# Kernel tuning notes

Hardware: AMD Instinct MI355X
Metric: run time of the kernel (lower is better)

## Reference

```python
import jax, jax.numpy as jnp
import numpy as np

COMMITMENT_COST = 0.25

def setup_inputs() -> dict:
    key = jax.random.key(0)
    k1, k2 = jax.random.split(key)
    z = jax.random.normal(k1, (8, 2048, 768), dtype=jnp.float32)
    # codebook initialized uniform(-1/K, 1/K) in the original; use same scale
    K = 2048
    emb = jax.random.uniform(k2, (K, 768), dtype=jnp.float32, minval=-1.0 / K, maxval=1.0 / K)
    return {"z": z, "emb": emb}

def reference(z, emb):
    B, S, D = z.shape
    z_flat = z.reshape(-1, D)                                   # [N, D]
    # squared-euclidean distances via expansion: ||z||^2 + ||e||^2 - 2 z e^T
    distances = (
        jnp.sum(z_flat * z_flat, axis=1, keepdims=True)
        + jnp.sum(emb * emb, axis=1)
        - 2.0 * jnp.matmul(z_flat, emb.T)
    )                                                           # [N, K]
    ids_flat = jnp.argmin(distances, axis=1)                    # [N]
    z_q = emb[ids_flat].reshape(z.shape)                        # gather + reshape
    concept_ids = ids_flat.reshape(B, S)
    # training path with use_ema=True: codebook_loss = 0, commitment term only.
    # NOTE: original (faithfully) computes mse(z.detach(), z_q) — grad flows to z_q.
    commitment_loss = jnp.mean((jax.lax.stop_gradient(z) - z_q) ** 2)
    vq_loss = COMMITMENT_COST * commitment_loss
    # straight-through estimator
    z_q_st = z + jax.lax.stop_gradient(z_q - z)
    return z_q_st, concept_ids, vq_loss
```

## Files before the change

kernel.cpp:

```cpp
#include <hip/hip_runtime.h>
#include <float.h>

typedef unsigned short ushort_t;
typedef unsigned int uint_t;

#define NROWS 16384
#define DDIM  768
#define KCODES 2048
#define NCB2   8
#define MARGIN 8e-4f

__device__ __forceinline__ ushort_t f2bf(float x) {
    uint_t u = __float_as_uint(x);
    uint_t r = (u + 0x7fffu + ((u >> 16) & 1u)) >> 16;
    return (ushort_t)r;
}

__device__ __forceinline__ uint_t fenc(float f) {
    uint_t u = __float_as_uint(f);
    return (u & 0x80000000u) ? ~u : (u | 0x80000000u);
}
__device__ __forceinline__ float fdec(uint_t k) {
    uint_t u = (k & 0x80000000u) ? (k ^ 0x80000000u) : ~k;
    return __uint_as_float(u);
}

__global__ void prep_kernel(const float* __restrict__ z, const float* __restrict__ emb,
                            float* __restrict__ ee, float* __restrict__ zz,
                            ushort_t* __restrict__ Zh, ushort_t* __restrict__ Eh,
                            float* __restrict__ out_loss) {
    const int b = blockIdx.x, t = threadIdx.x;
    if (b == 0 && t == 0) out_loss[0] = 0.f;
    if (b < KCODES) {
        const int c = b;
        const float* e = emb + (size_t)c * DDIM;
        float s = 0.f;
        for (int i = t; i < DDIM; i += 256) { float v = e[i]; s += v * v; }
        for (int off = 32; off; off >>= 1) s += __shfl_down(s, off);
        __shared__ float red[4];
        if ((t & 63) == 0) red[t >> 6] = s;
        __syncthreads();
        if (t == 0) ee[c] = red[0] + red[1] + red[2] + red[3];
        if (t < 192) {
            const float4 v = ((const float4*)e)[t];
            ushort4 h;
            h.x = f2bf(v.x); h.y = f2bf(v.y); h.z = f2bf(v.z); h.w = f2bf(v.w);
            ((ushort4*)(Eh + (size_t)c * DDIM))[t] = h;
        }
    } else {
        const int rb = b - KCODES;
        const int row = rb * 4 + (t >> 6);
        const int lane = t & 63;
        const float* zr = z + (size_t)row * DDIM;
        float s = 0.f;
        for (int i = lane; i < DDIM; i += 64) { float v = zr[i]; s += v * v; }
        for (int off = 32; off; off >>= 1) s += __shfl_down(s, off);
        if (lane == 0) zz[row] = s;
        const float4* zr4 = (const float4*)zr;
        ushort4* dh = (ushort4*)(Zh + (size_t)row * DDIM);
        #pragma unroll
        for (int j = 0; j < 3; ++j) {
            const int i4 = lane + 64 * j;
            const float4 v = zr4[i4];
            ushort4 h;
            h.x = f2bf(v.x); h.y = f2bf(v.y); h.z = f2bf(v.z); h.w = f2bf(v.w);
            dh[i4] = h;
        }
    }
}

typedef __attribute__((ext_vector_type(8))) short bf16x8;
typedef __attribute__((ext_vector_type(4))) float f32x4;

__device__ __forceinline__ int swz(int r) { return (r & 3) ^ ((r >> 2) & 3); }

#define RINGB 24576
#define CAPS  8

__global__ __launch_bounds__(256, 2)
void mfma_ring_kernel(const ushort_t* __restrict__ Ab, const ushort_t* __restrict__ Bb,
                      const float* __restrict__ ee, float* __restrict__ bmin,
                      float2* __restrict__ slots) {
    __shared__ __align__(16) char smem[3 * RINGB];
    uint_t* rowminU = (uint_t*)smem;
    int*    rcnt    = (int*)(smem + 512);
    float (*sval)[CAPS] = (float(*)[CAPS])(smem + 1024);
    int   (*sidx)[CAPS] = (int(*)[CAPS])(smem + 5120);

    const int t = threadIdx.x;
    const int w = t >> 6, l = t & 63;
    const int bx = blockIdx.x & 127;
    const int by = blockIdx.x >> 7;
    const int row0 = bx << 7;
    const int col0 = by << 8;

    f32x4 acc[4][8];
    #pragma unroll
    for (int i = 0; i < 4; ++i)
        #pragma unroll
        for (int j = 0; j < 8; ++j) acc[i][j] = (f32x4){0.f, 0.f, 0.f, 0.f};

    const int sri = l >> 2, slot = l & 3;
    const ushort_t* gA[2]; uint_t lA[2];
    #pragma unroll
    for (int q = 0; q < 2; ++q) {
        const int r0 = ((w << 1) + q) << 4;
        const int ra = r0 + sri;
        const int c  = slot ^ swz(ra);
        gA[q] = Ab + (size_t)(row0 + ra) * DDIM + (c << 3);
        lA[q] = r0 << 6;
    }
    const ushort_t* gB[4]; uint_t lB[4];
    #pragma unroll
    for (int q = 0; q < 4; ++q) {
        const int r0 = ((w << 2) + q) << 4;
        const int ra = r0 + sri;
        const int c  = slot ^ swz(ra);
        gB[q] = Bb + (size_t)(col0 + ra) * DDIM + (c << 3);
        lB[q] = 8192 + (r0 << 6);
    }

    const int rha = (w & 1) << 6;
    const int chb = (w >> 1) << 7;
    int aoff[4], boff[8];
    #pragma unroll
    for (int mi = 0; mi < 4; ++mi) {
        const int r = rha + (mi << 4) + (l & 15);
        const int sw = (l >> 4) ^ swz(r);
        aoff[mi] = (r << 6) + (sw << 4);
    }
    #pragma unroll
    for (int ni = 0; ni < 8; ++ni) {
        const int r = chb + (ni << 4) + (l & 15);
        const int sw = (l >> 4) ^ swz(r);
        boff[ni] = 8192 + (r << 6) + (sw << 4);
    }

#define STAGE(base_) do {                                                     \
        _Pragma("unroll")                                                     \
        for (int q = 0; q < 2; ++q) {                                         \
            __builtin_amdgcn_global_load_lds(                                 \
                (const __attribute__((address_space(1))) void*)gA[q],         \
                (__attribute__((address_space(3))) void*)(smem + (base_) + lA[q]), \
                16, 0, 0);                                                    \
            gA[q] += 32;                                                      \
        }                                                                     \
        _Pragma("unroll")                                                     \
        for (int q = 0; q < 4; ++q) {                                         \
            __builtin_amdgcn_global_load_lds(                                 \
                (const __attribute__((address_space(1))) void*)gB[q],         \
                (__attribute__((address_space(3))) void*)(smem + (base_) + lB[q]), \
                16, 0, 0);                                                    \
            gB[q] += 32;                                                      \
        }                                                                     \
    } while (0)

    STAGE(0);
    STAGE(RINGB);
    __syncthreads();

    int cur = 0, stg = 2;
    for (int kt = 0; kt < 24; ++kt) {
        if (kt < 22) STAGE((uint_t)stg * RINGB);

        const char* cb_ = smem + (uint_t)cur * RINGB;
        bf16x8 af[4], bfr[8];
        #pragma unroll
        for (int mi = 0; mi < 4; ++mi) af[mi] = *(const bf16x8*)(cb_ + aoff[mi]);
        #pragma unroll
        for (int ni = 0; ni < 8; ++ni) bfr[ni] = *(const bf16x8*)(cb_ + boff[ni]);

        __builtin_amdgcn_s_setprio(1);
        #pragma unroll
        for (int mi = 0; mi < 4; ++mi)
            #pragma unroll
            for (int ni = 0; ni < 8; ++ni)
                acc[mi][ni] = __builtin_amdgcn_mfma_f32_16x16x32_bf16(
                    af[mi], bfr[ni], acc[mi][ni], 0, 0, 0);
        __builtin_amdgcn_s_setprio(0);

        if (kt < 22) asm volatile("s_waitcnt vmcnt(6)" ::: "memory");
        else         asm volatile("s_waitcnt vmcnt(0)" ::: "memory");
        __builtin_amdgcn_sched_barrier(0);
        __builtin_amdgcn_s_barrier();
        __builtin_amdgcn_sched_barrier(0);

        cur = (cur == 2) ? 0 : cur + 1;
        stg = (stg == 2) ? 0 : stg + 1;
    }
#undef STAGE

    __syncthreads();

    if (t < 128) { rowminU[t] = 0xFFFFFFFFu; rcnt[t] = 0; }
    __syncthreads();

    float ecv[8];
    #pragma unroll
    for (int ni = 0; ni < 8; ++ni) ecv[ni] = ee[col0 + chb + (ni << 4) + (l & 15)];
    #pragma unroll
    for (int mi = 0; mi < 4; ++mi)
        #pragma unroll
        for (int ni = 0; ni < 8; ++ni)
            #pragma unroll
            for (int r = 0; r < 4; ++r)
                acc[mi][ni][r] = ecv[ni] - 2.0f * acc[mi][ni][r];

    #pragma unroll
    for (int mi = 0; mi < 4; ++mi)
        #pragma unroll
        for (int r = 0; r < 4; ++r) {
            float v = acc[mi][0][r];
            #pragma unroll
            for (int ni = 1; ni < 8; ++ni) v = fminf(v, acc[mi][ni][r]);
            v = fminf(v, __shfl_xor(v, 1));
            v = fminf(v, __shfl_xor(v, 2));
            v = fminf(v, __shfl_xor(v, 4));
            v = fminf(v, __shfl_xor(v, 8));
            if ((l & 15) == 0)
                atomicMin(&rowminU[rha + (mi << 4) + ((l >> 4) << 2) + r], fenc(v));
        }
    __syncthreads();

    #pragma unroll
    for (int mi = 0; mi < 4; ++mi)
        #pragma unroll
        for (int r = 0; r < 4; ++r) {
            const int m = rha + (mi << 4) + ((l >> 4) << 2) + r;
            const float lim = fdec(rowminU[m]) + MARGIN;
            #pragma unroll
            for (int ni = 0; ni < 8; ++ni) {
                const float vv = acc[mi][ni][r];
                if (vv <= lim) {
                    const int p = atomicAdd(&rcnt[m], 1);
                    if (p < CAPS) {
                        sval[m][p] = vv;
                        sidx[m][p] = col0 + chb + (ni << 4) + (l & 15);
                    }
                }
            }
        }
    __syncthreads();

    if (t < 128) {
        const int row = row0 + t;
        bmin[(size_t)by * NROWS + row] = fdec(rowminU[t]);
        const int n = rcnt[t] < CAPS ? rcnt[t] : CAPS;
        float2 rec[8];
        #pragma unroll
        for (int s2 = 0; s2 < 8; ++s2)
            rec[s2] = (s2 < n) ? make_float2(sval[t][s2], __int_as_float(sidx[t][s2]))
                               : make_float2(FLT_MAX, __int_as_float(0x7fffffff));
        float4* dst = (float4*)(slots + ((size_t)by * NROWS + row) * 8);
        dst[0] = make_float4(rec[0].x, rec[0].y, rec[1].x, rec[1].y);
        dst[1] = make_float4(rec[2].x, rec[2].y, rec[3].x, rec[3].y);
        dst[2] = make_float4(rec[4].x, rec[4].y, rec[5].x, rec[5].y);
        dst[3] = make_float4(rec[6].x, rec[6].y, rec[7].x, rec[7].y);
    }
}

__global__ __launch_bounds__(256)
void combine_select_gather(const float* __restrict__ bmin, const float2* __restrict__ slots,
                           const float* __restrict__ ee, const float* __restrict__ zz,
                           const float* __restrict__ z, const float* __restrict__ emb,
                           float* __restrict__ ids_f32, float* __restrict__ out0,
                           float* __restrict__ out_loss) {
    const int t = threadIdx.x;
    const int w = t >> 6;
    const int row = blockIdx.x * 4 + w;
    const int l = t & 63;

    float v = (l < NCB2) ? bmin[(size_t)l * NROWS + row] : FLT_MAX;
    v = fminf(v, __shfl_xor(v, 4));
    v = fminf(v, __shfl_xor(v, 2));
    v = fminf(v, __shfl_xor(v, 1));
    const float T = __shfl(v, 0) + MARGIN;

    const int blk = l >> 3;
    const int s0 = l & 7;
    const float2 a = slots[((size_t)blk * NROWS + row) * 8 + s0];

    unsigned long long m = __ballot(a.x <= T);

    const float* zr = z + (size_t)row * DDIM;
    int bi;
    if (__popcll(m) == 1) {
        bi = __float_as_int(__shfl(a.y, __ffsll(m) - 1));
    } else {
        const float zzr = zz[row];
        float bestd = FLT_MAX; int besti = 0x7fffffff;
        while (m) {
            const int j = __ffsll(m) - 1; m &= m - 1;
            const int idx = __float_as_int(__shfl(a.y, j));
            const float* er = emb + (size_t)idx * DDIM;
            float p = 0.f;
            #pragma unroll
            for (int k = 0; k < 12; ++k) p += zr[l + 64 * k] * er[l + 64 * k];
            for (int off = 32; off; off >>= 1) p += __shfl_down(p, off);
            if (l == 0) {
                const float t1 = zzr + ee[idx];
                const float d  = t1 - 2.0f * p;
                if (d < bestd || (d == bestd && idx < besti)) { bestd = d; besti = idx; }
            }
        }
        bi = __shfl(besti, 0);
    }
    if (l == 0) ids_f32[row] = (float)bi;

    const float4* zr4 = (const float4*)zr;
    const float4* er4 = (const float4*)(emb + (size_t)bi * DDIM);
    float4* o4 = (float4*)(out0 + (size_t)row * DDIM);
    float s = 0.f;
    #pragma unroll
    for (int j = 0; j < 3; ++j) {
        const int i4 = l + 64 * j;
        const float4 zv = zr4[i4];
        const float4 ev = er4[i4];
        float4 o;
        o.x = zv.x + (ev.x - zv.x); o.y = zv.y + (ev.y - zv.y);
        o.z = zv.z + (ev.z - zv.z); o.w = zv.w + (ev.w - zv.w);
        o4[i4] = o;
        const float dx = zv.x - ev.x, dy = zv.y - ev.y;
        const float dz = zv.z - ev.z, dw = zv.w - ev.w;
        s += dx * dx + dy * dy + dz * dz + dw * dw;
    }
    for (int off = 32; off; off >>= 1) s += __shfl_down(s, off);
    __shared__ float lred[4];
    if (l == 0) lred[w] = s;
    __syncthreads();
    if (t == 0) {
        const float tot = lred[0] + lred[1] + lred[2] + lred[3];
        atomicAdd(out_loss, tot * (0.25f / (float)((size_t)NROWS * DDIM)));
    }
}

__global__ void ee_kernel(const float* __restrict__ emb, float* __restrict__ ee) {
    int c = blockIdx.x;
    const float* e = emb + (size_t)c * DDIM;
    int t = threadIdx.x;
    float s = 0.f;
    for (int i = t; i < DDIM; i += 256) { float v = e[i]; s += v * v; }
    for (int off = 32; off; off >>= 1) s += __shfl_down(s, off);
    __shared__ float red[4];
    if ((t & 63) == 0) red[t >> 6] = s;
    __syncthreads();
    if (t == 0) ee[c] = red[0] + red[1] + red[2] + red[3];
}

__global__ void zz_kernel(const float* __restrict__ z, float* __restrict__ zz) {
    const int t = threadIdx.x;
    const int row = blockIdx.x * 4 + (t >> 6);
    const int lane = t & 63;
    const float* zr = z + (size_t)row * DDIM;
    float s = 0.f;
    for (int i = lane; i < DDIM; i += 64) { float v = zr[i]; s += v * v; }
    for (int off = 32; off; off >>= 1) s += __shfl_down(s, off);
    if (lane == 0) zz[row] = s;
}

#define BM 32
#define BN 128
#define BKS 32
#define SPLITC 2
#define CODES_PER_BLOCK (KCODES / SPLITC)
#define NCHUNK (CODES_PER_BLOCK / BN)
#define NSTAGE (DDIM / BKS)
#define APADR 33
#define BPADC 132

__global__ __launch_bounds__(256)
void argmin_kernel(const float* __restrict__ z, const float* __restrict__ emb,
                   const float* __restrict__ ee, const float* __restrict__ zz,
                   float* __restrict__ pval, int* __restrict__ pidx) {
    __shared__ float Af[BKS][APADR];
    __shared__ float Bf[BKS][BPADC];
    __shared__ float cval[BM][33];
    __shared__ int   cidx[BM][33];
    __shared__ float zzs[BM];
    const int t = threadIdx.x;
    const int part = blockIdx.x & (SPLITC - 1);
    const int rb = blockIdx.x >> 1;
    const int row0 = rb * BM;
    const int cbase = part * CODES_PER_BLOCK;
    const int tx = t & 31, ty = t >> 5;
    const int sr = t >> 3;
    const int sk = 4 * (t & 7);
    if (t < BM) zzs[t] = zz[row0 + t];
    float bv[4]; int bi[4];
    #pragma unroll
    for (int i = 0; i < 4; ++i) { bv[i] = FLT_MAX; bi[i] = 0x7fffffff; }
    const float* zt = z + (size_t)(row0 + sr) * DDIM;
    for (int chunk = 0; chunk < NCHUNK; ++chunk) {
        const int c0 = cbase + chunk * BN;
        const float* ebase = emb + (size_t)(c0 + sr) * DDIM;
        float acc[4][4];
        #pragma unroll
        for (int i = 0; i < 4; ++i)
            #pragma unroll
            for (int j = 0; j < 4; ++j) acc[i][j] = 0.f;
        float4 pa = *(const float4*)&zt[sk];
        float4 pb[4];
        #pragma unroll
        for (int m = 0; m < 4; ++m) pb[m] = *(const float4*)&ebase[(size_t)(32 * m) * DDIM + sk];
        for (int s = 0; s < NSTAGE; ++s) {
            __syncthreads();
            Af[sk + 0][sr] = pa.x; Af[sk + 1][sr] = pa.y;
            Af[sk + 2][sr] = pa.z; Af[sk + 3][sr] = pa.w;
            #pragma unroll
            for (int m = 0; m < 4; ++m) {
                Bf[sk + 0][sr + 32 * m] = pb[m].x;
                Bf[sk + 1][sr + 32 * m] = pb[m].y;
                Bf[sk + 2][sr + 32 * m] = pb[m].z;
                Bf[sk + 3][sr + 32 * m] = pb[m].w;
            }
            __syncthreads();
            if (s + 1 < NSTAGE) {
                const int k1 = (s + 1) * BKS + sk;
                pa = *(const float4*)&zt[k1];
                #pragma unroll
                for (int m = 0; m < 4; ++m)
                    pb[m] = *(const float4*)&ebase[(size_t)(32 * m) * DDIM + k1];
            }
            #pragma unroll
            for (int kk = 0; kk < BKS; ++kk) {
                const float4 a4 = *(const float4*)&Af[kk][4 * ty];
                const float4 b4 = *(const float4*)&Bf[kk][4 * tx];
                const float aa[4] = {a4.x, a4.y, a4.z, a4.w};
                const float bb[4] = {b4.x, b4.y, b4.z, b4.w};
                #pragma unroll
                for (int i = 0; i < 4; ++i)
                    #pragma unroll
                    for (int j = 0; j < 4; ++j) acc[i][j] += aa[i] * bb[j];
            }
        }
        const float4 e4 = *(const float4*)&ee[c0 + 4 * tx];
        const float eev[4] = {e4.x, e4.y, e4.z, e4.w};
        #pragma unroll
        for (int i = 0; i < 4; ++i) {
            const float zzr = zzs[4 * ty + i];
            #pragma unroll
            for (int j = 0; j < 4; ++j) {
                const int code = c0 + 4 * tx + j;
                const float t1 = zzr + eev[j];
                const float d  = t1 - 2.0f * acc[i][j];
                if (d < bv[i] || (d == bv[i] && code < bi[i])) { bv[i] = d; bi[i] = code; }
            }
        }
    }
    __syncthreads();
    #pragma unroll
    for (int i = 0; i < 4; ++i) { cval[4 * ty + i][tx] = bv[i]; cidx[4 * ty + i][tx] = bi[i]; }
    __syncthreads();
    if (t < BM) {
        float v = FLT_MAX; int id = 0x7fffffff;
        #pragma unroll
        for (int x = 0; x < 32; ++x) {
            const float cv = cval[t][x]; const int ci = cidx[t][x];
            if (cv < v || (cv == v && ci < id)) { v = cv; id = ci; }
        }
        pval[part * NROWS + row0 + t] = v;
        pidx[part * NROWS + row0 + t] = id;
    }
}

__global__ void combine_kernel(const float* __restrict__ pval, const int* __restrict__ pidx,
                               float* __restrict__ ids_f32) {
    const int r = blockIdx.x * 256 + threadIdx.x;
    float v = pval[r];           int id = pidx[r];
    const float v1 = pval[NROWS + r]; const int i1 = pidx[NROWS + r];
    if (v1 < v || (v1 == v && i1 < id)) { v = v1; id = i1; }
    ids_f32[r] = (float)id;
}

__global__ __launch_bounds__(256)
void gather_kernel(const float* __restrict__ z, const float* __restrict__ emb,
                   const float* __restrict__ ids_f32, float* __restrict__ out0,
                   float* __restrict__ part) {
    const int b = blockIdx.x;
    const int t = threadIdx.x;
    const int rl = t >> 4, c = t & 15;
    __shared__ int ids[16];
    if (t < 16) ids[t] = (int)ids_f32[b * 16 + t];
    __syncthreads();
    const int row = b * 16 + rl;
    const float4* zr = (const float4*)(z + (size_t)row * DDIM);
    float4* orow = (float4*)(out0 + (size_t)row * DDIM);
    const float4* er = (const float4*)(emb + (size_t)ids[rl] * DDIM);
    float s = 0.f;
    #pragma unroll
    for (int j = 0; j < 12; ++j) {
        const int i4 = c + 16 * j;
        const float4 zv = zr[i4];
        const float4 ev = er[i4];
        float4 o;
        o.x = zv.x + (ev.x - zv.x); o.y = zv.y + (ev.y - zv.y);
        o.z = zv.z + (ev.z - zv.z); o.w = zv.w + (ev.w - zv.w);
        orow[i4] = o;
        float dx = zv.x - ev.x, dy = zv.y - ev.y, dz = zv.z - ev.z, dw = zv.w - ev.w;
        s += dx * dx + dy * dy + dz * dz + dw * dw;
    }
    for (int off = 32; off; off >>= 1) s += __shfl_down(s, off);
    __shared__ float red[4];
    if ((t & 63) == 0) red[t >> 6] = s;
    __syncthreads();
    if (t == 0) part[b] = red[0] + red[1] + red[2] + red[3];
}

__global__ void loss_kernel(const float* __restrict__ part, float* __restrict__ out_loss) {
    const int t = threadIdx.x;
    double s = 0.0;
    for (int i = t; i < 1024; i += 256) s += (double)part[i];
    for (int off = 32; off; off >>= 1) s += __shfl_down(s, off);
    __shared__ double red[4];
    if ((t & 63) == 0) red[t >> 6] = s;
    __syncthreads();
    if (t == 0) {
        const double total = red[0] + red[1] + red[2] + red[3];
        out_loss[0] = (float)(0.25 * (total / (double)((size_t)NROWS * DDIM)));
    }
}

#define EE_OFF   0
#define ZZ_OFF   8192
#define EH_OFF   73728
#define ZH_OFF   (EH_OFF + (size_t)KCODES * DDIM * 2)
#define BMIN_OFF (ZH_OFF + (size_t)NROWS * DDIM * 2)
#define SLOT_OFF (BMIN_OFF + (size_t)NCB2 * NROWS * 4)
#define WS_NEED  (SLOT_OFF + (size_t)NCB2 * NROWS * 8 * 8)
#define PART_OFF 73728
#define PV_OFF   81920

extern "C" void kernel_launch(void* const* d_in, const int* in_sizes, int n_in,
                              void* d_out, int out_size, void* d_ws, size_t ws_size,
                              hipStream_t stream) {
    const float* z   = (const float*)d_in[0];
    const float* emb = (const float*)d_in[1];

    float* out0     = (float*)d_out;
    float* out_ids  = out0 + (size_t)NROWS * DDIM;
    float* out_loss = out_ids + NROWS;

    char* ws = (char*)d_ws;
    float* ee   = (float*)(ws + EE_OFF);
    float* zzws = (float*)(ws + ZZ_OFF);

    if (ws_size >= WS_NEED) {
        ushort_t* Eh   = (ushort_t*)(ws + EH_OFF);
        ushort_t* Zh   = (ushort_t*)(ws + ZH_OFF);
        float*    bmin = (float*)(ws + BMIN_OFF);
        float2*   slot = (float2*)(ws + SLOT_OFF);
        prep_kernel<<<KCODES + NROWS / 4, 256, 0, stream>>>(z, emb, ee, zzws, Zh, Eh, out_loss);
        mfma_ring_kernel<<<(NROWS / 128) * NCB2, 256, 0, stream>>>(Zh, Eh, ee, bmin, slot);
        combine_select_gather<<<NROWS / 4, 256, 0, stream>>>(bmin, slot, ee, zzws, z, emb,
                                                             out_ids, out0, out_loss);
    } else {
        float* part = (float*)(ws + PART_OFF);
        float* pval = (float*)(ws + PV_OFF);
        int*   pidx = (int*)(ws + PV_OFF + 131072);
        ee_kernel<<<KCODES, 256, 0, stream>>>(emb, ee);
        zz_kernel<<<NROWS / 4, 256, 0, stream>>>(z, zzws);
        argmin_kernel<<<(NROWS / BM) * SPLITC, 256, 0, stream>>>(z, emb, ee, zzws, pval, pidx);
        combine_kernel<<<NROWS / 256, 256, 0, stream>>>(pval, pidx, out_ids);
        gather_kernel<<<NROWS / 16, 256, 0, stream>>>(z, emb, out_ids, out0, part);
        loss_kernel<<<1, 256, 0, stream>>>(part, out_loss);
    }
}
```

Baseline: 242.0 us.

## Enlarge GEMM tile to 256x256 with 8 waves and 4-slot LDS ring

Replaces the 128x256-tile, 4-wave distance GEMM kernel with a 256x256-tile, 8-wave (512-thread) kernel whose waves are arranged 2x4, each computing 128x64. LDS becomes a 4-slot ring of 32 KB slots with prefetch distance two and a new XOR swizzle, and the next stage's loads are issued after the fragment reads. The larger tile halves the number of blocks and raises operand reuse per LDS byte, which cuts global and LDS traffic per MFMA. In exchange it uses 128 KB of LDS per block and more threads per block, which may limit occupancy and reduce the number of blocks available to fill the GPU.

```diff
diff --git a/kernel.cpp b/kernel.cpp
--- a/kernel.cpp
+++ b/kernel.cpp
@@ -72,177 +72,163 @@
 typedef __attribute__((ext_vector_type(8))) short bf16x8;
 typedef __attribute__((ext_vector_type(4))) float f32x4;
 
-__device__ __forceinline__ int swz(int r) { return (r & 3) ^ ((r >> 2) & 3); }
-
-#define RINGB 24576
+#define SLOT_SZ 32768
+#define BOFF_IN_SLOT 16384
+#define NSLICE 24
 #define CAPS  8
 
-__global__ __launch_bounds__(256, 2)
-void mfma_ring_kernel(const ushort_t* __restrict__ Ab, const ushort_t* __restrict__ Bb,
-                      const float* __restrict__ ee, float* __restrict__ bmin,
-                      float2* __restrict__ slots) {
-    __shared__ __align__(16) char smem[3 * RINGB];
+__global__ __launch_bounds__(512, 2)
+void mfma8_kernel(const ushort_t* __restrict__ Ab, const ushort_t* __restrict__ Bb,
+                  const float* __restrict__ ee, float* __restrict__ bmin,
+                  float2* __restrict__ slots) {
+    __shared__ __align__(16) char smem[4 * SLOT_SZ];
     uint_t* rowminU = (uint_t*)smem;
-    int*    rcnt    = (int*)(smem + 512);
-    float (*sval)[CAPS] = (float(*)[CAPS])(smem + 1024);
-    int   (*sidx)[CAPS] = (int(*)[CAPS])(smem + 5120);
+    int*    rcnt    = (int*)(smem + 1024);
+    float (*sval)[CAPS] = (float(*)[CAPS])(smem + 2048);
+    int   (*sidx)[CAPS] = (int(*)[CAPS])(smem + 10240);
 
     const int t = threadIdx.x;
     const int w = t >> 6, l = t & 63;
-    const int bx = blockIdx.x & 127;
-    const int by = blockIdx.x >> 7;
-    const int row0 = bx << 7;
+    const int bx = blockIdx.x & 63;
+    const int by = blockIdx.x >> 6;
+    const int row0 = bx << 8;
     const int col0 = by << 8;
 
-    f32x4 acc[4][8];
-    #pragma unroll
-    for (int i = 0; i < 4; ++i)
-        #pragma unroll
-        for (int j = 0; j < 8; ++j) acc[i][j] = (f32x4){0.f, 0.f, 0.f, 0.f};
-
-    const int sri = l >> 2, slot = l & 3;
-    const ushort_t* gA[2]; uint_t lA[2];
+    f32x4 acc[8][4];
+    #pragma unroll
+    for (int i = 0; i < 8; ++i)
+        #pragma unroll
+        for (int j = 0; j < 4; ++j) acc[i][j] = (f32x4){0.f, 0.f, 0.f, 0.f};
+
+    size_t gAoff[2], gBoff[2]; uint_t ldsA[2], ldsB[2];
     #pragma unroll
     for (int q = 0; q < 2; ++q) {
-        const int r0 = ((w << 1) + q) << 4;
-        const int ra = r0 + sri;
-        const int c  = slot ^ swz(ra);
-        gA[q] = Ab + (size_t)(row0 + ra) * DDIM + (c << 3);
-        lA[q] = r0 << 6;
-    }
-    const ushort_t* gB[4]; uint_t lB[4];
-    #pragma unroll
-    for (int q = 0; q < 4; ++q) {
-        const int r0 = ((w << 2) + q) << 4;
-        const int ra = r0 + sri;
-        const int c  = slot ^ swz(ra);
-        gB[q] = Bb + (size_t)(col0 + ra) * DDIM + (c << 3);
-        lB[q] = 8192 + (r0 << 6);
-    }
-
-    const int rha = (w & 1) << 6;
-    const int chb = (w >> 1) << 7;
-    int aoff[4], boff[8];
-    #pragma unroll
-    for (int mi = 0; mi < 4; ++mi) {
-        const int r = rha + (mi << 4) + (l & 15);
-        const int sw = (l >> 4) ^ swz(r);
-        aoff[mi] = (r << 6) + (sw << 4);
-    }
-    #pragma unroll
-    for (int ni = 0; ni < 8; ++ni) {
-        const int r = chb + (ni << 4) + (l & 15);
-        const int sw = (l >> 4) ^ swz(r);
-        boff[ni] = 8192 + (r << 6) + (sw << 4);
-    }
-
-#define STAGE(base_) do {                                                     \
-        _Pragma("unroll")                                                     \
-        for (int q = 0; q < 2; ++q) {                                         \
-            __builtin_amdgcn_global_load_lds(                                 \
-                (const __attribute__((address_space(1))) void*)gA[q],         \
-                (__attribute__((address_space(3))) void*)(smem + (base_) + lA[q]), \
-                16, 0, 0);                                                    \
-            gA[q] += 32;                                                      \
-        }                                                                     \
-        _Pragma("unroll")                                                     \
-        for (int q = 0; q < 4; ++q) {                                         \
-            __builtin_amdgcn_global_load_lds(                                 \
-                (const __attribute__((address_space(1))) void*)gB[q],         \
-                (__attribute__((address_space(3))) void*)(smem + (base_) + lB[q]), \
-                16, 0, 0);                                                    \
-            gB[q] += 32;                                                      \
-        }                                                                     \
+        const int r = (w * 2 + q) * 16 + (l >> 2);
+        const int gs = (l & 3) ^ ((r >> 1) & 3);
+        gAoff[q] = (size_t)(row0 + r) * DDIM + gs * 8;
+        gBoff[q] = (size_t)(col0 + r) * DDIM + gs * 8;
+        ldsA[q] = (w * 2 + q) * 1024;
+        ldsB[q] = BOFF_IN_SLOT + (w * 2 + q) * 1024;
+    }
+
+#define STAGE(Sg_) do {                                                        \
+        const uint_t sb_ = (uint_t)((Sg_) & 3) * SLOT_SZ;                      \
+        const int ko_ = (Sg_) * 32;                                            \
+        _Pragma("unroll")                                                      \
+        for (int q = 0; q < 2; ++q)                                            \
+            __builtin_amdgcn_global_load_lds(                                  \
+                (const __attribute__((address_space(1))) void*)(Ab + gAoff[q] + ko_), \
+                (__attribute__((address_space(3))) void*)(smem + sb_ + ldsA[q]), \
+                16, 0, 0);                                                     \
+        _Pragma("unroll")                                                      \
+        for (int q = 0; q < 2; ++q)                                            \
+            __builtin_amdgcn_global_load_lds(                                  \
+                (const __attribute__((address_space(1))) void*)(Bb + gBoff[q] + ko_), \
+                (__attribute__((address_space(3))) void*)(smem + sb_ + ldsB[q]), \
+                16, 0, 0);                                                     \
     } while (0)
 
+    const int g = l >> 4, lr = l & 15;
+    const int wm = w >> 2, wn = w & 3;
+    int aoff[8], boff[4];
+    #pragma unroll
+    for (int mi = 0; mi < 8; ++mi) {
+        const int r = wm * 128 + mi * 16 + lr;
+        aoff[mi] = r * 64 + ((g ^ ((r >> 1) & 3)) << 4);
+    }
+    #pragma unroll
+    for (int ni = 0; ni < 4; ++ni) {
+        const int r = wn * 64 + ni * 16 + lr;
+        boff[ni] = BOFF_IN_SLOT + r * 64 + ((g ^ ((r >> 1) & 3)) << 4);
+    }
+
     STAGE(0);
-    STAGE(RINGB);
-    __syncthreads();
-
-    int cur = 0, stg = 2;
-    for (int kt = 0; kt < 24; ++kt) {
-        if (kt < 22) STAGE((uint_t)stg * RINGB);
-
-        const char* cb_ = smem + (uint_t)cur * RINGB;
-        bf16x8 af[4], bfr[8];
-        #pragma unroll
-        for (int mi = 0; mi < 4; ++mi) af[mi] = *(const bf16x8*)(cb_ + aoff[mi]);
-        #pragma unroll
-        for (int ni = 0; ni < 8; ++ni) bfr[ni] = *(const bf16x8*)(cb_ + boff[ni]);
+    STAGE(1);
+    asm volatile("s_waitcnt vmcnt(4)" ::: "memory");
+    __builtin_amdgcn_sched_barrier(0);
+    __builtin_amdgcn_s_barrier();
+    __builtin_amdgcn_sched_barrier(0);
+
+    for (int S = 0; S < NSLICE; ++S) {
+        const char* sb = smem + (uint_t)(S & 3) * SLOT_SZ;
+        bf16x8 af[8], bfr[4];
+        #pragma unroll
+        for (int mi = 0; mi < 8; ++mi) af[mi] = *(const bf16x8*)(sb + aoff[mi]);
+        #pragma unroll
+        for (int ni = 0; ni < 4; ++ni) bfr[ni] = *(const bf16x8*)(sb + boff[ni]);
+
+        if (S < NSLICE - 2) STAGE(S + 2);
 
         __builtin_amdgcn_s_setprio(1);
         #pragma unroll
-        for (int mi = 0; mi < 4; ++mi)
-            #pragma unroll
-            for (int ni = 0; ni < 8; ++ni)
+        for (int mi = 0; mi < 8; ++mi)
+            #pragma unroll
+            for (int ni = 0; ni < 4; ++ni)
                 acc[mi][ni] = __builtin_amdgcn_mfma_f32_16x16x32_bf16(
                     af[mi], bfr[ni], acc[mi][ni], 0, 0, 0);
         __builtin_amdgcn_s_setprio(0);
 
-        if (kt < 22) asm volatile("s_waitcnt vmcnt(6)" ::: "memory");
-        else         asm volatile("s_waitcnt vmcnt(0)" ::: "memory");
+        if (S < NSLICE - 2)       asm volatile("s_waitcnt vmcnt(4)" ::: "memory");
+        else if (S == NSLICE - 2) asm volatile("s_waitcnt vmcnt(0)" ::: "memory");
         __builtin_amdgcn_sched_barrier(0);
         __builtin_amdgcn_s_barrier();
         __builtin_amdgcn_sched_barrier(0);
-
-        cur = (cur == 2) ? 0 : cur + 1;
-        stg = (stg == 2) ? 0 : stg + 1;
     }
 #undef STAGE
 
     __syncthreads();
 
-    if (t < 128) { rowminU[t] = 0xFFFFFFFFu; rcnt[t] = 0; }
-    __syncthreads();
-
-    float ecv[8];
-    #pragma unroll
-    for (int ni = 0; ni < 8; ++ni) ecv[ni] = ee[col0 + chb + (ni << 4) + (l & 15)];
-    #pragma unroll
-    for (int mi = 0; mi < 4; ++mi)
-        #pragma unroll
-        for (int ni = 0; ni < 8; ++ni)
+    if (t < 256) { rowminU[t] = 0xFFFFFFFFu; rcnt[t] = 0; }
+    __syncthreads();
+
+    float ecv[4];
+    #pragma unroll
+    for (int ni = 0; ni < 4; ++ni) ecv[ni] = ee[col0 + wn * 64 + (ni << 4) + lr];
+    #pragma unroll
+    for (int mi = 0; mi < 8; ++mi)
+        #pragma unroll
+        for (int ni = 0; ni < 4; ++ni)
             #pragma unroll
             for (int r = 0; r < 4; ++r)
                 acc[mi][ni][r] = ecv[ni] - 2.0f * acc[mi][ni][r];
 
     #pragma unroll
-    for (int mi = 0; mi < 4; ++mi)
+    for (int mi = 0; mi < 8; ++mi)
         #pragma unroll
         for (int r = 0; r < 4; ++r) {
             float v = acc[mi][0][r];
             #pragma unroll
-            for (int ni = 1; ni < 8; ++ni) v = fminf(v, acc[mi][ni][r]);
+            for (int ni = 1; ni < 4; ++ni) v = fminf(v, acc[mi][ni][r]);
             v = fminf(v, __shfl_xor(v, 1));
             v = fminf(v, __shfl_xor(v, 2));
             v = fminf(v, __shfl_xor(v, 4));
             v = fminf(v, __shfl_xor(v, 8));
-            if ((l & 15) == 0)
-                atomicMin(&rowminU[rha + (mi << 4) + ((l >> 4) << 2) + r], fenc(v));
-        }
-    __syncthreads();
-
-    #pragma unroll
-    for (int mi = 0; mi < 4; ++mi)
+            if (lr == 0)
+                atomicMin(&rowminU[wm * 128 + (mi << 4) + (g << 2) + r], fenc(v));
+        }
+    __syncthreads();
+
+    #pragma unroll
+    for (int mi = 0; mi < 8; ++mi)
         #pragma unroll
         for (int r = 0; r < 4; ++r) {
-            const int m = rha + (mi << 4) + ((l >> 4) << 2) + r;
+            const int m = wm * 128 + (mi << 4) + (g << 2) + r;
             const float lim = fdec(rowminU[m]) + MARGIN;
             #pragma unroll
-            for (int ni = 0; ni < 8; ++ni) {
+            for (int ni = 0; ni < 4; ++ni) {
                 const float vv = acc[mi][ni][r];
                 if (vv <= lim) {
                     const int p = atomicAdd(&rcnt[m], 1);
                     if (p < CAPS) {
                         sval[m][p] = vv;
-                        sidx[m][p] = col0 + chb + (ni << 4) + (l & 15);
+                        sidx[m][p] = col0 + wn * 64 + (ni << 4) + lr;
                     }
                 }
             }
         }
     __syncthreads();
 
-    if (t < 128) {
+    if (t < 256) {
         const int row = row0 + t;
         bmin[(size_t)by * NROWS + row] = fdec(rowminU[t]);
         const int n = rcnt[t] < CAPS ? rcnt[t] : CAPS;
@@ -550,7 +536,7 @@
         float*    bmin = (float*)(ws + BMIN_OFF);
         float2*   slot = (float2*)(ws + SLOT_OFF);
         prep_kernel<<<KCODES + NROWS / 4, 256, 0, stream>>>(z, emb, ee, zzws, Zh, Eh, out_loss);
-        mfma_ring_kernel<<<(NROWS / 128) * NCB2, 256, 0, stream>>>(Zh, Eh, ee, bmin, slot);
+        mfma8_kernel<<<(NROWS / 256) * NCB2, 512, 0, stream>>>(Zh, Eh, ee, bmin, slot);
         combine_select_gather<<<NROWS / 4, 256, 0, stream>>>(bmin, slot, ee, zzws, z, emb,
                                                              out_ids, out0, out_loss);
     } else {
```

After: 241.9 us. No clear change (-0.0%).
